# Kernel optimization log

Measured on AMD Instinct MI355X. Metric: run time of the kernel, lower is better.

## Reference

```python
import jax, jax.numpy as jnp
import numpy as np

TAU = 0.11
ALPHA = 32.0  # scale
EPS = 1e-12   # torch F.normalize eps


def _l2norm(t):
    n = jnp.linalg.norm(t, axis=-1, keepdims=True)
    return t / jnp.maximum(n, EPS)


def setup_inputs() -> dict:
    key = jax.random.key(0)
    k1, k2, k3, k4 = jax.random.split(key, 4)
    B, N, C, D = 8192, 100000, 1000, 768
    return {
        "x": jax.random.normal(k1, (B, D), dtype=jnp.float32),
        "support_features": jax.random.normal(k2, (N, D), dtype=jnp.float32),
        "support_labels": jax.random.randint(k3, (N,), 0, C),
        "W": jax.random.normal(k4, (D, D), dtype=jnp.float32) * 0.02,
        "b": jnp.zeros((D,), dtype=jnp.float32),
        "num_classes": C,
    }


def reference(x, support_features, support_labels, W, b, num_classes):
    def adapter(t):
        h = t @ W.T + b              # nn.Linear(D, D)
        return jax.nn.silu(h) + t    # SiLU + residual (use_zifa)

    embeddings = _l2norm(adapter(x))                      # (B, D)
    support_key = _l2norm(adapter(support_features))      # (N, D)

    # per-class mean prototype via one segment-sum pass
    sums = jax.ops.segment_sum(support_key, support_labels, num_segments=num_classes)  # (C, D)
    counts = jax.ops.segment_sum(
        jnp.ones((support_key.shape[0],), dtype=support_key.dtype),
        support_labels, num_segments=num_classes)          # (C,)
    means = sums / jnp.maximum(counts, 1.0)[:, None]
    prototypes = jnp.where((counts > 0)[:, None], _l2norm(means), 0.0)  # (C, D)

    # mvrec logits: exp(-(alpha - alpha*cos)) / tau
    cos_sim = embeddings @ prototypes.T                    # (B, C)
    logits = jnp.exp(-(ALPHA - ALPHA * cos_sim)) / max(TAU, 1e-9)
    predicts = jax.nn.softmax(logits, axis=-1)
    return predicts, logits, embeddings
```

## Files before the change

### kernel.cpp

```cpp
#include <hip/hip_runtime.h>
#include <hip/hip_bf16.h>
#include <stdint.h>

typedef __bf16 v8bf __attribute__((ext_vector_type(8)));
typedef float  v4f  __attribute__((ext_vector_type(4)));
typedef unsigned short u16;
typedef unsigned int   u32;

#define B_ROWS   8192
#define N_SUP    100000
#define N_CLS    1000
#define CPAD     1024
#define DIM      768
#define MSUP_PAD 100352

__device__ __forceinline__ u16 f2bf(float f) {
    union { float f; u32 u; } v; v.f = f;
    u32 r = 0x7FFFu + ((v.u >> 16) & 1u);
    return (u16)((v.u + r) >> 16);
}
__device__ __forceinline__ float bf2f(u16 b) {
    union { u32 u; float f; } v; v.u = ((u32)b) << 16; return v.f;
}
__device__ __forceinline__ void glds16(const void* g, void* l) {
    __builtin_amdgcn_global_load_lds((const __attribute__((address_space(1))) u32*)g,
                                     (__attribute__((address_space(3))) u32*)l, 16, 0, 0);
}

__device__ __forceinline__ float block_sum(float v, float* red) {
    #pragma unroll
    for (int o = 32; o > 0; o >>= 1) v += __shfl_down(v, o);
    int wv = threadIdx.x >> 6, ln = threadIdx.x & 63;
    if (ln == 0) red[wv] = v;
    __syncthreads();
    return red[0] + red[1] + red[2] + red[3];
}
__device__ __forceinline__ float block_max(float v, float* red) {
    #pragma unroll
    for (int o = 32; o > 0; o >>= 1) v = fmaxf(v, __shfl_down(v, o));
    int wv = threadIdx.x >> 6, ln = threadIdx.x & 63;
    if (ln == 0) red[wv] = v;
    __syncthreads();
    return fmaxf(fmaxf(red[0], red[1]), fmaxf(red[2], red[3]));
}

__device__ __forceinline__ int xcd_swizzle(void) {
    const int nwg = gridDim.x * gridDim.y;
    const int bid = blockIdx.y * gridDim.x + blockIdx.x;
    const int q = nwg >> 3;
    return (bid & 7) * q + (bid >> 3);
}

__global__ __launch_bounds__(256)
void conv_pad_kernel(const float* __restrict__ in, u16* __restrict__ out,
                     int n_real) {
    #pragma unroll
    for (int s = 0; s < 3; s++) {
        size_t f4 = (size_t)blockIdx.x * 768 + s * 256 + threadIdx.x;
        int row = (int)(f4 / 192);
        size_t eb = f4 * 4;
        ushort4 o;
        if (row < n_real) {
            float4 v = *(const float4*)(in + eb);
            o.x = f2bf(v.x); o.y = f2bf(v.y); o.z = f2bf(v.z); o.w = f2bf(v.w);
        } else {
            o.x = 0; o.y = 0; o.z = 0; o.w = 0;
        }
        *(ushort4*)(out + eb) = o;
    }
}

__global__ __launch_bounds__(256)
void adapter_gemm_kernel(const u16* __restrict__ A, const u16* __restrict__ Wb,
                         const float* __restrict__ bias,
                         u16* __restrict__ val, float* __restrict__ ss) {
    __shared__ u16 As[2][128 * 64];
    __shared__ u16 Bs[2][128 * 64];

    const int tid  = threadIdx.x;
    const int wave = tid >> 6, lane = tid & 63;
    const int fq = lane >> 4, fr = lane & 15;

    const int swz = xcd_swizzle();
    const int blk_m = (swz / gridDim.x) * 128;
    const int blk_n = (swz % gridDim.x) * 128;

    const int wm = (wave & 1) * 64, wn = (wave >> 1) * 64;

    v4f acc[4][4];
    #pragma unroll
    for (int i = 0; i < 4; i++)
        #pragma unroll
        for (int j = 0; j < 4; j++) acc[i][j] = (v4f){0.f, 0.f, 0.f, 0.f};

    const int rb = lane >> 3;
    const int cb = (lane & 7) * 8;
    const u16* gA = A  + (size_t)(blk_m + wave * 8 + rb) * DIM + cb;
    const u16* gB = Wb + (size_t)(blk_n + wave * 8 + rb) * DIM + cb;

    auto STAGE = [&](int buf, int k0) {
        #pragma unroll
        for (int p = 0; p < 4; p++) {
            glds16(gA + (size_t)p * 32 * DIM + k0, &As[buf][p * 2048 + wave * 512]);
            glds16(gB + (size_t)p * 32 * DIM + k0, &Bs[buf][p * 2048 + wave * 512]);
        }
    };
    auto COMPUTE = [&](int buf) {
        #pragma unroll
        for (int ks = 0; ks < 2; ks++) {
            const int kk = ks * 32;
            v8bf af[4], bfr[4];
            #pragma unroll
            for (int i = 0; i < 4; i++) {
                af[i]  = *(const v8bf*)(&As[buf][(wm + i * 16 + fr) * 64 + kk + fq * 8]);
                bfr[i] = *(const v8bf*)(&Bs[buf][(wn + i * 16 + fr) * 64 + kk + fq * 8]);
            }
            #pragma unroll
            for (int i = 0; i < 4; i++)
                #pragma unroll
                for (int j = 0; j < 4; j++)
                    acc[i][j] = __builtin_amdgcn_mfma_f32_16x16x32_bf16(
                        af[i], bfr[j], acc[i][j], 0, 0, 0);
        }
    };

    STAGE(0, 0);
    __syncthreads();
    int cur = 0;
    for (int k0 = 64; k0 < DIM; k0 += 64) {
        STAGE(cur ^ 1, k0);
        COMPUTE(cur);
        __syncthreads();
        cur ^= 1;
    }
    COMPUTE(cur);

    #pragma unroll
    for (int i = 0; i < 4; i++) {
        int r0 = blk_m + wm + i * 16 + fq * 4;
        float ssp[4] = {0.f, 0.f, 0.f, 0.f};
        #pragma unroll
        for (int j = 0; j < 4; j++) {
            int col = blk_n + wn + j * 16 + fr;
            float bv = bias[col];
            #pragma unroll
            for (int r2 = 0; r2 < 4; r2++) {
                int gr = r0 + r2;
                float h = acc[i][j][r2] + bv;
                float t = bf2f(A[(size_t)gr * DIM + col]);
                float v = h / (1.f + __expf(-h)) + t;
                ssp[r2] += v * v;
                val[(size_t)gr * DIM + col] = f2bf(v);
            }
        }
        #pragma unroll
        for (int r2 = 0; r2 < 4; r2++) {
            float s = ssp[r2];
            s += __shfl_xor(s, 1); s += __shfl_xor(s, 2);
            s += __shfl_xor(s, 4); s += __shfl_xor(s, 8);
            if (fr == 0) atomicAdd(&ss[r0 + r2], s);
        }
    }
}

__global__ void norm_x_kernel(const u16* __restrict__ val, const float* __restrict__ ss,
                              float* __restrict__ emb, u16* __restrict__ emb_bf) {
    int row = blockIdx.x;
    float sc = 1.f / fmaxf(sqrtf(ss[row]), 1e-12f);
    size_t b = (size_t)row * DIM + threadIdx.x * 4;
    ushort4 v = *(const ushort4*)(val + b);
    float4 o;
    o.x = bf2f(v.x) * sc; o.y = bf2f(v.y) * sc;
    o.z = bf2f(v.z) * sc; o.w = bf2f(v.w) * sc;
    *(float4*)(emb + b) = o;
    ushort4 ob; ob.x = f2bf(o.x); ob.y = f2bf(o.y); ob.z = f2bf(o.z); ob.w = f2bf(o.w);
    *(ushort4*)(emb_bf + b) = ob;
}

__global__ __launch_bounds__(256)
void proto_kernel(const u16* __restrict__ val_bf, const float* __restrict__ ss,
                  const int* __restrict__ labels, u16* __restrict__ proto_bf) {
    __shared__ int queue[256];
    __shared__ int qn;
    __shared__ float red[4];
    const int cls = blockIdx.x, tid = threadIdx.x;
    if (tid == 0) qn = 0;
    __syncthreads();
    for (int i4 = tid; i4 < N_SUP / 4; i4 += 256) {
        int4 L = *(const int4*)(labels + i4 * 4);
        if (L.x == cls) queue[atomicAdd(&qn, 1) & 255] = i4 * 4;
        if (L.y == cls) queue[atomicAdd(&qn, 1) & 255] = i4 * 4 + 1;
        if (L.z == cls) queue[atomicAdd(&qn, 1) & 255] = i4 * 4 + 2;
        if (L.w == cls) queue[atomicAdd(&qn, 1) & 255] = i4 * 4 + 3;
    }
    __syncthreads();
    const int n = qn < 256 ? qn : 256;
    float a0 = 0.f, a1 = 0.f, a2 = 0.f;
    for (int e = 0; e < n; e++) {
        int row = queue[e];
        float sc = 1.f / fmaxf(sqrtf(ss[row]), 1e-12f);
        const u16* vr = val_bf + (size_t)row * DIM;
        a0 += bf2f(vr[tid])       * sc;
        a1 += bf2f(vr[tid + 256]) * sc;
        a2 += bf2f(vr[tid + 512]) * sc;
    }
    float inv_cnt = 1.f / fmaxf((float)n, 1.f);
    float m0 = a0 * inv_cnt, m1 = a1 * inv_cnt, m2 = a2 * inv_cnt;
    float tot = block_sum(m0 * m0 + m1 * m1 + m2 * m2, red);
    float sc2 = (n > 0) ? 1.f / fmaxf(sqrtf(tot), 1e-12f) : 0.f;
    size_t b = (size_t)cls * DIM;
    proto_bf[b + tid]       = f2bf(m0 * sc2);
    proto_bf[b + tid + 256] = f2bf(m1 * sc2);
    proto_bf[b + tid + 512] = f2bf(m2 * sc2);
}

__global__ __launch_bounds__(256)
void cos_gemm_kernel(const u16* __restrict__ Ab, const u16* __restrict__ Pb,
                     float* __restrict__ logits) {
    __shared__ u16 As[2][128 * 64];
    __shared__ u16 Bs[2][128 * 64];
    const int tid  = threadIdx.x;
    const int wave = tid >> 6, lane = tid & 63;
    const int fq = lane >> 4, fr = lane & 15;

    const int swz = xcd_swizzle();
    const int blk_m = (swz / gridDim.x) * 128;
    const int blk_n = (swz % gridDim.x) * 128;

    const int wm = (wave & 1) * 64, wn = (wave >> 1) * 64;

    v4f acc[4][4];
    #pragma unroll
    for (int i = 0; i < 4; i++)
        #pragma unroll
        for (int j = 0; j < 4; j++) acc[i][j] = (v4f){0.f, 0.f, 0.f, 0.f};

    const int rb = lane >> 3;
    const int cb = (lane & 7) * 8;
    const u16* gA = Ab + (size_t)(blk_m + wave * 8 + rb) * DIM + cb;
    const u16* gB = Pb + (size_t)(blk_n + wave * 8 + rb) * DIM + cb;

    auto STAGE = [&](int buf, int k0) {
        #pragma unroll
        for (int p = 0; p < 4; p++) {
            glds16(gA + (size_t)p * 32 * DIM + k0, &As[buf][p * 2048 + wave * 512]);
            glds16(gB + (size_t)p * 32 * DIM + k0, &Bs[buf][p * 2048 + wave * 512]);
        }
    };
    auto COMPUTE = [&](int buf) {
        #pragma unroll
        for (int ks = 0; ks < 2; ks++) {
            const int kk = ks * 32;
            v8bf af[4], bfr[4];
            #pragma unroll
            for (int i = 0; i < 4; i++) {
                af[i]  = *(const v8bf*)(&As[buf][(wm + i * 16 + fr) * 64 + kk + fq * 8]);
                bfr[i] = *(const v8bf*)(&Bs[buf][(wn + i * 16 + fr) * 64 + kk + fq * 8]);
            }
            #pragma unroll
            for (int i = 0; i < 4; i++)
                #pragma unroll
                for (int j = 0; j < 4; j++)
                    acc[i][j] = __builtin_amdgcn_mfma_f32_16x16x32_bf16(
                        af[i], bfr[j], acc[i][j], 0, 0, 0);
        }
    };

    STAGE(0, 0);
    __syncthreads();
    int cur = 0;
    for (int k0 = 64; k0 < DIM; k0 += 64) {
        STAGE(cur ^ 1, k0);
        COMPUTE(cur);
        __syncthreads();
        cur ^= 1;
    }
    COMPUTE(cur);

    #pragma unroll
    for (int i = 0; i < 4; i++) {
        int r0 = blk_m + wm + i * 16 + fq * 4;
        #pragma unroll
        for (int j = 0; j < 4; j++) {
            int col = blk_n + wn + j * 16 + fr;
            if (col < N_CLS) {
                #pragma unroll
                for (int r2 = 0; r2 < 4; r2++) {
                    float c = acc[i][j][r2];
                    logits[(size_t)(r0 + r2) * N_CLS + col] =
                        __expf(32.0f * (c - 1.0f)) * (1.0f / 0.11f);
                }
            }
        }
    }
}

__global__ __launch_bounds__(256)
void softmax_kernel(const float* __restrict__ logits, float* __restrict__ predicts) {
    __shared__ float redm[4];
    __shared__ float reds[4];
    int row = blockIdx.x, tid = threadIdx.x;
    const float* lr = logits + (size_t)row * N_CLS;
    float4 lg = make_float4(-1.f, -1.f, -1.f, -1.f);
    bool act = tid < N_CLS / 4;
    if (act) lg = *(const float4*)(lr + tid * 4);
    float mx = fmaxf(fmaxf(lg.x, lg.y), fmaxf(lg.z, lg.w));
    float mxt = block_max(mx, redm);
    float4 e = make_float4(0.f, 0.f, 0.f, 0.f);
    float s = 0.f;
    if (act) {
        e.x = __expf(lg.x - mxt); e.y = __expf(lg.y - mxt);
        e.z = __expf(lg.z - mxt); e.w = __expf(lg.w - mxt);
        s = e.x + e.y + e.z + e.w;
    }
    float st = block_sum(s, reds);
    float inv = 1.f / st;
    if (act) {
        float4 o; o.x = e.x * inv; o.y = e.y * inv; o.z = e.z * inv; o.w = e.w * inv;
        *(float4*)(predicts + (size_t)row * N_CLS + tid * 4) = o;
    }
}

extern "C" void kernel_launch(void* const* d_in, const int* in_sizes, int n_in,
                              void* d_out, int out_size, void* d_ws, size_t ws_size,
                              hipStream_t stream) {
    const float* x      = (const float*)d_in[0];
    const float* sup    = (const float*)d_in[1];
    const int*   labels = (const int*)d_in[2];
    const float* W      = (const float*)d_in[3];
    const float* bias   = (const float*)d_in[4];

    float* predicts = (float*)d_out;
    float* logits   = predicts + (size_t)B_ROWS * N_CLS;
    float* emb      = logits + (size_t)B_ROWS * N_CLS;

    char* ws = (char*)d_ws;
    size_t off = 0;
    u16*   w_bf     = (u16*)(ws + off);   off += (size_t)DIM * DIM * 2;
    u16*   x_bf     = (u16*)(ws + off);   off += (size_t)B_ROWS * DIM * 2;
    u16*   sup_bf   = (u16*)(ws + off);   off += (size_t)MSUP_PAD * DIM * 2;
    u16*   val_x    = (u16*)(ws + off);   off += (size_t)B_ROWS * DIM * 2;
    u16*   val_sup  = (u16*)(ws + off);   off += (size_t)MSUP_PAD * DIM * 2;
    u16*   emb_bf   = (u16*)(ws + off);   off += (size_t)B_ROWS * DIM * 2;
    u16*   proto_bf = (u16*)(ws + off);   off += (size_t)CPAD * DIM * 2;
    float* ss_sup   = (float*)(ws + off); off += (size_t)MSUP_PAD * 4;
    float* ss_x     = (float*)(ws + off); off += (size_t)B_ROWS * 4;

    hipMemsetAsync(ss_sup, 0, ((size_t)MSUP_PAD + B_ROWS) * 4, stream);

    conv_pad_kernel<<<DIM / 4,      256, 0, stream>>>(W,   w_bf,   DIM);
    conv_pad_kernel<<<B_ROWS / 4,   256, 0, stream>>>(x,   x_bf,   B_ROWS);
    conv_pad_kernel<<<MSUP_PAD / 4, 256, 0, stream>>>(sup, sup_bf, N_SUP);

    adapter_gemm_kernel<<<dim3(DIM / 128, B_ROWS / 128), 256, 0, stream>>>(
        x_bf, w_bf, bias, val_x, ss_x);
    adapter_gemm_kernel<<<dim3(DIM / 128, MSUP_PAD / 128), 256, 0, stream>>>(
        sup_bf, w_bf, bias, val_sup, ss_sup);

    norm_x_kernel<<<B_ROWS, 192, 0, stream>>>(val_x, ss_x, emb, emb_bf);

    proto_kernel<<<CPAD, 256, 0, stream>>>(val_sup, ss_sup, labels, proto_bf);

    cos_gemm_kernel<<<dim3(CPAD / 128, B_ROWS / 128), 256, 0, stream>>>(
        emb_bf, proto_bf, logits);
    softmax_kernel<<<B_ROWS, 256, 0, stream>>>(logits, predicts);
}
```

Measured before the change: 907.9 us.

## Fuse fp32-to-bf16 conversion into adapter GEMM, prebuild class queues, swizzle LDS

The adapter GEMM now loads the fp32 activations directly, converts them to bf16 in registers and writes them to an XOR-swizzled LDS tile. This removes the separate conversion passes over x and the support set, and the bf16 copies they wrote and read back. A new build_queues kernel groups support rows by label with a single atomic pass, replacing the full 100k-label scan that every prototype block used to do. The prototype accumulation loop is unrolled by four. Both GEMMs also get swizzled LDS reads and s_setprio around the MFMA section, and f2bf now uses the native bf16 cast. In exchange, the A tile passes through registers, which adds register pressure, and the GEMM residual is read from fp32 global memory.

```diff
diff --git a/kernel.cpp b/kernel.cpp
--- a/kernel.cpp
+++ b/kernel.cpp
@@ -3,6 +3,7 @@
 #include <stdint.h>
 
 typedef __bf16 v8bf __attribute__((ext_vector_type(8)));
+typedef __bf16 v4bf __attribute__((ext_vector_type(4)));
 typedef float  v4f  __attribute__((ext_vector_type(4)));
 typedef unsigned short u16;
 typedef unsigned int   u32;
@@ -15,9 +16,8 @@
 #define MSUP_PAD 100352
 
 __device__ __forceinline__ u16 f2bf(float f) {
-    union { float f; u32 u; } v; v.f = f;
-    u32 r = 0x7FFFu + ((v.u >> 16) & 1u);
-    return (u16)((v.u + r) >> 16);
+    __bf16 b = (__bf16)f;
+    union { __bf16 b; u16 u; } v; v.b = b; return v.u;
 }
 __device__ __forceinline__ float bf2f(u16 b) {
     union { u32 u; float f; } v; v.u = ((u32)b) << 16; return v.f;
@@ -71,8 +71,19 @@
 }
 
 __global__ __launch_bounds__(256)
-void adapter_gemm_kernel(const u16* __restrict__ A, const u16* __restrict__ Wb,
-                         const float* __restrict__ bias,
+void build_queues_kernel(const int* __restrict__ labels, int* __restrict__ qcnt,
+                         int* __restrict__ qlist) {
+    int i = blockIdx.x * 256 + threadIdx.x;
+    if (i < N_SUP) {
+        int l = labels[i];
+        int p = atomicAdd(&qcnt[l], 1);
+        if (p < 256) qlist[l * 256 + p] = i;
+    }
+}
+
+__global__ __launch_bounds__(256)
+void adapter_gemm_kernel(const float* __restrict__ A, const u16* __restrict__ Wb,
+                         const float* __restrict__ bias, int n_real,
                          u16* __restrict__ val, float* __restrict__ ss) {
     __shared__ u16 As[2][128 * 64];
     __shared__ u16 Bs[2][128 * 64];
@@ -93,43 +104,74 @@
         #pragma unroll
         for (int j = 0; j < 4; j++) acc[i][j] = (v4f){0.f, 0.f, 0.f, 0.f};
 
-    const int rb = lane >> 3;
-    const int cb = (lane & 7) * 8;
-    const u16* gA = A  + (size_t)(blk_m + wave * 8 + rb) * DIM + cb;
-    const u16* gB = Wb + (size_t)(blk_n + wave * 8 + rb) * DIM + cb;
-
-    auto STAGE = [&](int buf, int k0) {
-        #pragma unroll
-        for (int p = 0; p < 4; p++) {
-            glds16(gA + (size_t)p * 32 * DIM + k0, &As[buf][p * 2048 + wave * 512]);
+    const int rb  = lane >> 3;
+    const int cbs = ((lane & 7) ^ rb) * 8;
+    const u16* gB = Wb + (size_t)(blk_n + wave * 8 + rb) * DIM + cbs;
+
+    const int arow = tid >> 4;
+    const int af4  = tid & 15;
+
+    float4 ra[8];
+    auto LOADA = [&](int k0) {
+        #pragma unroll
+        for (int p = 0; p < 8; p++) {
+            int grow = blk_m + p * 16 + arow;
+            if (grow < n_real)
+                ra[p] = *(const float4*)(A + (size_t)grow * DIM + k0 + af4 * 4);
+            else
+                ra[p] = make_float4(0.f, 0.f, 0.f, 0.f);
+        }
+    };
+    auto WRITEA = [&](int buf) {
+        #pragma unroll
+        for (int p = 0; p < 8; p++) {
+            int row = p * 16 + arow;
+            int off = row * 64 + (((af4 >> 1) ^ (row & 7)) * 8) + (af4 & 1) * 4;
+            v4bf o;
+            o[0] = (__bf16)ra[p].x; o[1] = (__bf16)ra[p].y;
+            o[2] = (__bf16)ra[p].z; o[3] = (__bf16)ra[p].w;
+            *(v4bf*)(&As[buf][off]) = o;
+        }
+    };
+    auto STAGEB = [&](int buf, int k0) {
+        #pragma unroll
+        for (int p = 0; p < 4; p++)
             glds16(gB + (size_t)p * 32 * DIM + k0, &Bs[buf][p * 2048 + wave * 512]);
-        }
     };
     auto COMPUTE = [&](int buf) {
         #pragma unroll
         for (int ks = 0; ks < 2; ks++) {
-            const int kk = ks * 32;
+            const int gbase = ks * 4;
             v8bf af[4], bfr[4];
             #pragma unroll
             for (int i = 0; i < 4; i++) {
-                af[i]  = *(const v8bf*)(&As[buf][(wm + i * 16 + fr) * 64 + kk + fq * 8]);
-                bfr[i] = *(const v8bf*)(&Bs[buf][(wn + i * 16 + fr) * 64 + kk + fq * 8]);
+                int rowa = wm + i * 16 + fr;
+                int rowb = wn + i * 16 + fr;
+                int g    = (gbase + fq) ^ (fr & 7);
+                af[i]  = *(const v8bf*)(&As[buf][rowa * 64 + g * 8]);
+                bfr[i] = *(const v8bf*)(&Bs[buf][rowb * 64 + g * 8]);
             }
+            __builtin_amdgcn_s_setprio(1);
             #pragma unroll
             for (int i = 0; i < 4; i++)
                 #pragma unroll
                 for (int j = 0; j < 4; j++)
                     acc[i][j] = __builtin_amdgcn_mfma_f32_16x16x32_bf16(
                         af[i], bfr[j], acc[i][j], 0, 0, 0);
-        }
-    };
-
-    STAGE(0, 0);
+            __builtin_amdgcn_s_setprio(0);
+        }
+    };
+
+    LOADA(0);
+    STAGEB(0, 0);
+    WRITEA(0);
     __syncthreads();
     int cur = 0;
     for (int k0 = 64; k0 < DIM; k0 += 64) {
-        STAGE(cur ^ 1, k0);
+        LOADA(k0);
+        STAGEB(cur ^ 1, k0);
         COMPUTE(cur);
+        WRITEA(cur ^ 1);
         __syncthreads();
         cur ^= 1;
     }
@@ -147,7 +189,7 @@
             for (int r2 = 0; r2 < 4; r2++) {
                 int gr = r0 + r2;
                 float h = acc[i][j][r2] + bv;
-                float t = bf2f(A[(size_t)gr * DIM + col]);
+                float t = (gr < n_real) ? A[(size_t)gr * DIM + col] : 0.f;
                 float v = h / (1.f + __expf(-h)) + t;
                 ssp[r2] += v * v;
                 val[(size_t)gr * DIM + col] = f2bf(v);
@@ -179,25 +221,34 @@
 
 __global__ __launch_bounds__(256)
 void proto_kernel(const u16* __restrict__ val_bf, const float* __restrict__ ss,
-                  const int* __restrict__ labels, u16* __restrict__ proto_bf) {
-    __shared__ int queue[256];
-    __shared__ int qn;
+                  const int* __restrict__ qcnt, const int* __restrict__ qlist,
+                  u16* __restrict__ proto_bf) {
     __shared__ float red[4];
     const int cls = blockIdx.x, tid = threadIdx.x;
-    if (tid == 0) qn = 0;
-    __syncthreads();
-    for (int i4 = tid; i4 < N_SUP / 4; i4 += 256) {
-        int4 L = *(const int4*)(labels + i4 * 4);
-        if (L.x == cls) queue[atomicAdd(&qn, 1) & 255] = i4 * 4;
-        if (L.y == cls) queue[atomicAdd(&qn, 1) & 255] = i4 * 4 + 1;
-        if (L.z == cls) queue[atomicAdd(&qn, 1) & 255] = i4 * 4 + 2;
-        if (L.w == cls) queue[atomicAdd(&qn, 1) & 255] = i4 * 4 + 3;
-    }
-    __syncthreads();
-    const int n = qn < 256 ? qn : 256;
+    int n = qcnt[cls]; if (n > 256) n = 256;
+    const int* ql = qlist + (size_t)cls * 256;
     float a0 = 0.f, a1 = 0.f, a2 = 0.f;
-    for (int e = 0; e < n; e++) {
-        int row = queue[e];
+    int e = 0;
+    for (; e + 4 <= n; e += 4) {
+        int r0 = ql[e], r1 = ql[e + 1], r2 = ql[e + 2], r3 = ql[e + 3];
+        float s0 = 1.f / fmaxf(sqrtf(ss[r0]), 1e-12f);
+        float s1 = 1.f / fmaxf(sqrtf(ss[r1]), 1e-12f);
+        float s2 = 1.f / fmaxf(sqrtf(ss[r2]), 1e-12f);
+        float s3 = 1.f / fmaxf(sqrtf(ss[r3]), 1e-12f);
+        const u16* p0 = val_bf + (size_t)r0 * DIM;
+        const u16* p1 = val_bf + (size_t)r1 * DIM;
+        const u16* p2 = val_bf + (size_t)r2 * DIM;
+        const u16* p3 = val_bf + (size_t)r3 * DIM;
+        u16 x00 = p0[tid], x01 = p0[tid + 256], x02 = p0[tid + 512];
+        u16 x10 = p1[tid], x11 = p1[tid + 256], x12 = p1[tid + 512];
+        u16 x20 = p2[tid], x21 = p2[tid + 256], x22 = p2[tid + 512];
+        u16 x30 = p3[tid], x31 = p3[tid + 256], x32 = p3[tid + 512];
+        a0 += bf2f(x00) * s0 + bf2f(x10) * s1 + bf2f(x20) * s2 + bf2f(x30) * s3;
+        a1 += bf2f(x01) * s0 + bf2f(x11) * s1 + bf2f(x21) * s2 + bf2f(x31) * s3;
+        a2 += bf2f(x02) * s0 + bf2f(x12) * s1 + bf2f(x22) * s2 + bf2f(x32) * s3;
+    }
+    for (; e < n; e++) {
+        int row = ql[e];
         float sc = 1.f / fmaxf(sqrtf(ss[row]), 1e-12f);
         const u16* vr = val_bf + (size_t)row * DIM;
         a0 += bf2f(vr[tid])       * sc;
@@ -235,10 +286,10 @@
         #pragma unroll
         for (int j = 0; j < 4; j++) acc[i][j] = (v4f){0.f, 0.f, 0.f, 0.f};
 
-    const int rb = lane >> 3;
-    const int cb = (lane & 7) * 8;
-    const u16* gA = Ab + (size_t)(blk_m + wave * 8 + rb) * DIM + cb;
-    const u16* gB = Pb + (size_t)(blk_n + wave * 8 + rb) * DIM + cb;
+    const int rb  = lane >> 3;
+    const int cbs = ((lane & 7) ^ rb) * 8;
+    const u16* gA = Ab + (size_t)(blk_m + wave * 8 + rb) * DIM + cbs;
+    const u16* gB = Pb + (size_t)(blk_n + wave * 8 + rb) * DIM + cbs;
 
     auto STAGE = [&](int buf, int k0) {
         #pragma unroll
@@ -250,19 +301,24 @@
     auto COMPUTE = [&](int buf) {
         #pragma unroll
         for (int ks = 0; ks < 2; ks++) {
-            const int kk = ks * 32;
+            const int gbase = ks * 4;
             v8bf af[4], bfr[4];
             #pragma unroll
             for (int i = 0; i < 4; i++) {
-                af[i]  = *(const v8bf*)(&As[buf][(wm + i * 16 + fr) * 64 + kk + fq * 8]);
-                bfr[i] = *(const v8bf*)(&Bs[buf][(wn + i * 16 + fr) * 64 + kk + fq * 8]);
+                int rowa = wm + i * 16 + fr;
+                int rowb = wn + i * 16 + fr;
+                int g    = (gbase + fq) ^ (fr & 7);
+                af[i]  = *(const v8bf*)(&As[buf][rowa * 64 + g * 8]);
+                bfr[i] = *(const v8bf*)(&Bs[buf][rowb * 64 + g * 8]);
             }
+            __builtin_amdgcn_s_setprio(1);
             #pragma unroll
             for (int i = 0; i < 4; i++)
                 #pragma unroll
                 for (int j = 0; j < 4; j++)
                     acc[i][j] = __builtin_amdgcn_mfma_f32_16x16x32_bf16(
                         af[i], bfr[j], acc[i][j], 0, 0, 0);
+            __builtin_amdgcn_s_setprio(0);
         }
     };
 
@@ -337,29 +393,28 @@
     char* ws = (char*)d_ws;
     size_t off = 0;
     u16*   w_bf     = (u16*)(ws + off);   off += (size_t)DIM * DIM * 2;
-    u16*   x_bf     = (u16*)(ws + off);   off += (size_t)B_ROWS * DIM * 2;
-    u16*   sup_bf   = (u16*)(ws + off);   off += (size_t)MSUP_PAD * DIM * 2;
     u16*   val_x    = (u16*)(ws + off);   off += (size_t)B_ROWS * DIM * 2;
     u16*   val_sup  = (u16*)(ws + off);   off += (size_t)MSUP_PAD * DIM * 2;
     u16*   emb_bf   = (u16*)(ws + off);   off += (size_t)B_ROWS * DIM * 2;
     u16*   proto_bf = (u16*)(ws + off);   off += (size_t)CPAD * DIM * 2;
     float* ss_sup   = (float*)(ws + off); off += (size_t)MSUP_PAD * 4;
     float* ss_x     = (float*)(ws + off); off += (size_t)B_ROWS * 4;
-
-    hipMemsetAsync(ss_sup, 0, ((size_t)MSUP_PAD + B_ROWS) * 4, stream);
-
-    conv_pad_kernel<<<DIM / 4,      256, 0, stream>>>(W,   w_bf,   DIM);
-    conv_pad_kernel<<<B_ROWS / 4,   256, 0, stream>>>(x,   x_bf,   B_ROWS);
-    conv_pad_kernel<<<MSUP_PAD / 4, 256, 0, stream>>>(sup, sup_bf, N_SUP);
+    int*   qcnt     = (int*)(ws + off);   off += (size_t)CPAD * 4;
+    int*   qlist    = (int*)(ws + off);   off += (size_t)N_CLS * 256 * 4;
+
+    hipMemsetAsync(ss_sup, 0, ((size_t)MSUP_PAD + B_ROWS + CPAD) * 4, stream);
+
+    conv_pad_kernel<<<DIM / 4, 256, 0, stream>>>(W, w_bf, DIM);
+    build_queues_kernel<<<(N_SUP + 255) / 256, 256, 0, stream>>>(labels, qcnt, qlist);
 
     adapter_gemm_kernel<<<dim3(DIM / 128, B_ROWS / 128), 256, 0, stream>>>(
-        x_bf, w_bf, bias, val_x, ss_x);
+        x, w_bf, bias, B_ROWS, val_x, ss_x);
     adapter_gemm_kernel<<<dim3(DIM / 128, MSUP_PAD / 128), 256, 0, stream>>>(
-        sup_bf, w_bf, bias, val_sup, ss_sup);
+        sup, w_bf, bias, N_SUP, val_sup, ss_sup);
 
     norm_x_kernel<<<B_ROWS, 192, 0, stream>>>(val_x, ss_x, emb, emb_bf);
 
-    proto_kernel<<<CPAD, 256, 0, stream>>>(val_sup, ss_sup, labels, proto_bf);
+    proto_kernel<<<CPAD, 256, 0, stream>>>(val_sup, ss_sup, qcnt, qlist, proto_bf);
 
     cos_gemm_kernel<<<dim3(CPAD / 128, B_ROWS / 128), 256, 0, stream>>>(
         emb_bf, proto_bf, logits);
```

After: 1.305 ms. 1.44x slower.
